# Performance work log

Measured on AMD Instinct MI355X. Metric: run time of the kernel, lower is better.

Reference implementation:

```python
import jax, jax.numpy as jnp
import numpy as np

H = 8  # num_heads, fixed in the module


def setup_inputs() -> dict:
    key = jax.random.key(0)
    ks = jax.random.split(key, 26)
    C = 256          # hidden_dim
    K = 16           # num_corners
    B = 8            # images
    P = 64           # proposals per image
    N = B * P        # total proposals
    Hf = Wf = 14     # feature map HxW (T = 196 keys per proposal)
    Hq = Wq = 10     # query grid (S = 100 queries)
    s = 1.0 / np.sqrt(C)

    def w(k, shape):
        return jax.random.normal(k, shape, jnp.float32) * s

    return {
        "features": jax.random.normal(ks[0], (N, C, Hf, Wf), jnp.float32),
        "query_features": jax.random.normal(ks[1], (B, C, Hq, Wq), jnp.float32),
        # self-attention params (torch MHA: y = x @ W.T + b)
        "wq_s": w(ks[2], (C, C)), "wk_s": w(ks[3], (C, C)), "wv_s": w(ks[4], (C, C)),
        "bq_s": jnp.zeros((C,), jnp.float32), "bk_s": jnp.zeros((C,), jnp.float32), "bv_s": jnp.zeros((C,), jnp.float32),
        "wo_s": w(ks[5], (C, C)), "bo_s": jnp.zeros((C,), jnp.float32),
        # cross-attention params
        "wq_c": w(ks[6], (C, C)), "wk_c": w(ks[7], (C, C)), "wv_c": w(ks[8], (C, C)),
        "bq_c": jnp.zeros((C,), jnp.float32), "bk_c": jnp.zeros((C,), jnp.float32), "bv_c": jnp.zeros((C,), jnp.float32),
        "wo_c": w(ks[9], (C, C)), "bo_c": jnp.zeros((C,), jnp.float32),
        # polygon MLP head
        "w1": w(ks[10], (C, C)), "b1": jnp.zeros((C,), jnp.float32),
        "w2": w(ks[11], (2 * K, C)), "b2": jnp.zeros((2 * K,), jnp.float32),
        # score head
        "ws": w(ks[12], (1, C)), "bs": jnp.zeros((1,), jnp.float32),
    }


def _forward(features, query_features,
             wq_s, wk_s, wv_s, bq_s, bk_s, bv_s, wo_s, bo_s,
             wq_c, wk_c, wv_c, bq_c, bk_c, bv_c, wo_c, bo_c,
             w1, b1, w2, b2, ws, bs):
    B, C = query_features.shape[0], query_features.shape[1]
    dh = C // H
    scale = 1.0 / jnp.sqrt(jnp.asarray(dh, jnp.float32))

    # query_features: (B,C,Hq,Wq) -> (S,B,C)
    qf = query_features.reshape(B, C, -1).transpose(2, 0, 1)
    S = qf.shape[0]

    # ---- self-attention over queries ----
    q = (qf @ wq_s.T + bq_s).reshape(S, B, H, dh)
    k = (qf @ wk_s.T + bk_s).reshape(S, B, H, dh)
    v = (qf @ wv_s.T + bv_s).reshape(S, B, H, dh)
    att = jax.nn.softmax(jnp.einsum('sbhd,tbhd->bhst', q, k) * scale, axis=-1)
    qsa = jnp.einsum('bhst,tbhd->sbhd', att, v).reshape(S, B, C) @ wo_s.T + bo_s  # (S,B,C)

    # features: (N,C,Hf,Wf) -> (B,P,T,C) with T=Hf*Wf, P=N//B
    N = features.shape[0]
    P = N // B
    feats = features.reshape(N, C, -1).transpose(0, 2, 1).reshape(B, P, -1, C)

    # ---- cross-attention: same (S,C) query broadcast over P proposals ----
    qc = (qsa @ wq_c.T + bq_c).reshape(S, B, H, dh)
    kc = (feats @ wk_c.T + bk_c).reshape(B, P, -1, H, dh)
    vc = (feats @ wv_c.T + bv_c).reshape(B, P, -1, H, dh)
    sc = jnp.einsum('sbhd,bpthd->bphst', qc, kc) * scale  # (B,P,H,S,T)
    a = jax.nn.softmax(sc, axis=-1)
    o = jnp.einsum('bphst,bpthd->bpshd', a, vc).reshape(B, P, S, C) @ wo_c.T + bo_c  # (B,P,S,C)

    # ---- heads, then mean over the S query positions ----
    h1 = jax.nn.relu(o @ w1.T + b1)
    polygons = (h1 @ w2.T + b2).mean(axis=2).reshape(N, -1)          # (N, 2K)
    scores = jax.nn.sigmoid(o @ ws.T + bs).mean(axis=2).reshape(N, 1)  # (N, 1)
    return polygons, scores


def reference(features, query_features,
              wq_s, wk_s, wv_s, bq_s, bk_s, bv_s, wo_s, bo_s,
              wq_c, wk_c, wv_c, bq_c, bk_c, bv_c, wo_c, bo_c,
              w1, b1, w2, b2, ws, bs):
    return _forward(features, query_features,
                    wq_s, wk_s, wv_s, bq_s, bk_s, bv_s, wo_s, bo_s,
                    wq_c, wk_c, wv_c, bq_c, bk_c, bv_c, wo_c, bo_c,
                    w1, b1, w2, b2, ws, bs)
```

## Files before the change

kernel.cpp:

```cpp
#include <hip/hip_runtime.h>
#include <hip/hip_bf16.h>


typedef __attribute__((ext_vector_type(8))) short bf16x8;
typedef __attribute__((ext_vector_type(4))) float f32x4;

__device__ __forceinline__ float bf2f(ushort u) {
    union { float f; uint u32; } v; v.u32 = ((uint)u) << 16; return v.f;
}
__device__ __forceinline__ ushort f2bf(float f) {
    union { float f; uint u; } v; v.f = f;
    uint r = v.u + 0x7FFF + ((v.u >> 16) & 1);
    return (ushort)(r >> 16);
}
__device__ __forceinline__ uint pk2(float a, float b) {
    __hip_bfloat162 h = __float22bfloat162_rn(make_float2(a, b));
    union { __hip_bfloat162 h2; uint u; } c; c.h2 = h; return c.u;
}
__device__ __forceinline__ f32x4 MFMA(bf16x8 a, bf16x8 b, f32x4 c) {
    return __builtin_amdgcn_mfma_f32_16x16x32_bf16(a, b, c, 0, 0, 0);
}

#define SCALE_DH 0.17677669529663687f

#define TOTALW (2337 * 256)
#define QCPN   (8 * 8 * 112 * 32)
#define NBIAS  2337

__global__ void prep_kernel(const float* w0, const float* w1_, const float* w2_,
                            const float* w3, const float* w4, const float* w5,
                            const float* w6, const float* w7, const float* w8,
                            const float* w9, const float* w10,
                            const float* b0, const float* b1_, const float* b2_,
                            const float* b3, const float* b4, const float* b5,
                            const float* b6, const float* b7, const float* b8,
                            const float* b9, const float* b10,
                            ushort* wbf, float* bias, ushort* qcp)
{
    for (size_t i = blockIdx.x * blockDim.x + threadIdx.x;
         i < (size_t)TOTALW + QCPN + NBIAS; i += (size_t)gridDim.x * blockDim.x) {
        if (i < TOTALW) {
            int row = (int)(i >> 8), col = (int)(i & 255);
            const float* sp; int base;
            if      (row < 256)  { sp = w0;  base = 0; }
            else if (row < 512)  { sp = w1_; base = 256; }
            else if (row < 768)  { sp = w2_; base = 512; }
            else if (row < 1024) { sp = w3;  base = 768; }
            else if (row < 1280) { sp = w4;  base = 1024; }
            else if (row < 1536) { sp = w5;  base = 1280; }
            else if (row < 1792) { sp = w6;  base = 1536; }
            else if (row < 2048) { sp = w7;  base = 1792; }
            else if (row < 2304) { sp = w8;  base = 2048; }
            else if (row < 2336) { sp = w9;  base = 2304; }
            else                 { sp = w10; base = 2336; }
            wbf[i] = f2bf(sp[(size_t)(row - base) * 256 + col]);
        } else if (i < (size_t)TOTALW + QCPN) {
            qcp[i - TOTALW] = 0;
        } else {
            int idx = (int)(i - TOTALW - QCPN);
            const float* sp; int base;
            if      (idx < 256)  { sp = b0;  base = 0; }
            else if (idx < 512)  { sp = b1_; base = 256; }
            else if (idx < 768)  { sp = b2_; base = 512; }
            else if (idx < 1024) { sp = b3;  base = 768; }
            else if (idx < 1280) { sp = b4;  base = 1024; }
            else if (idx < 1536) { sp = b5;  base = 1280; }
            else if (idx < 1792) { sp = b6;  base = 1536; }
            else if (idx < 2048) { sp = b7;  base = 1792; }
            else if (idx < 2304) { sp = b8;  base = 2048; }
            else if (idx < 2336) { sp = b9;  base = 2304; }
            else                 { sp = b10; base = 2336; }
            bias[idx] = sp[idx - base];
        }
    }
}

__global__ __launch_bounds__(256)
void wcomb(const float* wq_c, const float* wo_s, const float* bq_c,
           const float* bo_s, const float* bo_c, const float* wsc,
           const float* bs, ushort* wbf, float* bias)
{
    __shared__ float row[256];
    int i = blockIdx.x, k = threadIdx.x;
    row[k] = wq_c[(size_t)i * 256 + k];
    __syncthreads();
    float acc = 0.f;
    for (int j = 0; j < 256; ++j)
        acc = fmaf(row[j], wo_s[(size_t)j * 256 + k], acc);
    wbf[(size_t)(1024 + i) * 256 + k] = f2bf(acc);
    if (k == 0) {
        float s = bq_c[i];
        for (int j = 0; j < 256; ++j) s += row[j] * bo_s[j];
        bias[1024 + i] = s;
    }
    if (i == 0 && k == 1) {
        float s = bs[0];
        for (int j = 0; j < 256; ++j) s += bo_c[j] * wsc[j];
        bias[2336] = s;
    }
}

template<int ASRC, int GS, int EPI>
__global__ __launch_bounds__(256)
void gemm_rows(const void* Aptr, const ushort* Wall, const float* Ball,
               ushort* Out, int M, int Wrow0, int Brow0, int ldo)
{
    __shared__ ushort As[64 * 40];
    __shared__ ushort Bs[128 * 40];
    int tid = threadIdx.x;
    int lane = tid & 63, w = tid >> 6;
    int lr = lane & 15, lg = lane >> 4;
    int r0 = blockIdx.x * 64;
    int j0 = blockIdx.y * 128;

    f32x4 acc[4][2];
    #pragma unroll
    for (int mt = 0; mt < 4; ++mt)
        #pragma unroll
        for (int nt = 0; nt < 2; ++nt) { f32x4 z = {0.f,0.f,0.f,0.f}; acc[mt][nt] = z; }

    for (int ks = 0; ks < 8; ++ks) {
        int c0 = ks * 32;
        {
            int i = tid >> 2, q = tid & 3;
            int r = r0 + i;
            if (ASRC == 0) {
                uint4 v = make_uint4(0u,0u,0u,0u);
                if (r < M) v = *(const uint4*)((const ushort*)Aptr + (size_t)r * 256 + c0 + q * 8);
                *(uint4*)(&As[i * 40 + q * 8]) = v;
            } else {
                uint u[4] = {0u,0u,0u,0u};
                if (r < M) {
                    int g = r / GS, o = r - g * GS;
                    const float* src = (const float*)Aptr + (size_t)g * 256 * GS + o;
                    #pragma unroll
                    for (int k2 = 0; k2 < 4; ++k2) {
                        ushort a0 = f2bf(src[(size_t)(c0 + q * 8 + 2 * k2)     * GS]);
                        ushort a1 = f2bf(src[(size_t)(c0 + q * 8 + 2 * k2 + 1) * GS]);
                        u[k2] = (uint)a0 | ((uint)a1 << 16);
                    }
                }
                *(uint4*)(&As[i * 40 + q * 8]) = make_uint4(u[0], u[1], u[2], u[3]);
            }
        }
        {
            int jj = tid >> 1, half = tid & 1;
            const ushort* src = Wall + (size_t)(Wrow0 + j0 + jj) * 256 + c0 + half * 16;
            ushort* dst = &Bs[jj * 40 + half * 16];
            *(uint4*)(dst)     = *(const uint4*)(src);
            *(uint4*)(dst + 8) = *(const uint4*)(src + 8);
        }
        __syncthreads();
        bf16x8 bfr[2];
        #pragma unroll
        for (int nt = 0; nt < 2; ++nt)
            bfr[nt] = *(const bf16x8*)(&Bs[(w * 32 + nt * 16 + lr) * 40 + lg * 8]);
        #pragma unroll
        for (int mt = 0; mt < 4; ++mt) {
            bf16x8 afr = *(const bf16x8*)(&As[(mt * 16 + lr) * 40 + lg * 8]);
            acc[mt][0] = MFMA(afr, bfr[0], acc[mt][0]);
            acc[mt][1] = MFMA(afr, bfr[1], acc[mt][1]);
        }
        __syncthreads();
    }
    #pragma unroll
    for (int mt = 0; mt < 4; ++mt) {
        #pragma unroll
        for (int nt = 0; nt < 2; ++nt) {
            int jc = j0 + w * 32 + nt * 16 + lr;
            float bias = Ball[Brow0 + jc];
            #pragma unroll
            for (int rg = 0; rg < 4; ++rg) {
                int r = r0 + mt * 16 + lg * 4 + rg;
                if (r >= M) continue;
                float vv = acc[mt][nt][rg] + bias;
                if (EPI == 0) {
                    Out[(size_t)r * ldo + jc] = f2bf(vv);
                } else {
                    int b = r / 100, s = r - b * 100;
                    int h = jc >> 5, d = jc & 31;
                    Out[(((size_t)(b * 8 + h)) * 112 + s) * 32 + d] = f2bf(vv * SCALE_DH);
                }
            }
        }
    }
}

__global__ __launch_bounds__(128)
void self_attn(const ushort* qkv, ushort* sav)
{
    __shared__ float kls[100][33];
    __shared__ float vls[100][33];
    __shared__ float sls[100][101];
    int bh = blockIdx.x; int b = bh >> 3, h = bh & 7;
    int tid = threadIdx.x;
    for (int idx = tid; idx < 100 * 32; idx += 128) {
        int t = idx >> 5, d = idx & 31;
        kls[t][d] = bf2f(qkv[((size_t)(b * 100 + t)) * 768 + 256 + h * 32 + d]);
        vls[t][d] = bf2f(qkv[((size_t)(b * 100 + t)) * 768 + 512 + h * 32 + d]);
    }
    __syncthreads();
    if (tid < 100) {
        int s = tid;
        float q[32];
        #pragma unroll
        for (int d = 0; d < 32; ++d)
            q[d] = bf2f(qkv[((size_t)(b * 100 + s)) * 768 + h * 32 + d]) * SCALE_DH;
        float mx = -1e30f;
        for (int t = 0; t < 100; ++t) {
            float sc = 0.f;
            #pragma unroll
            for (int d = 0; d < 32; ++d) sc += q[d] * kls[t][d];
            sls[s][t] = sc; mx = fmaxf(mx, sc);
        }
        float sum = 0.f;
        for (int t = 0; t < 100; ++t) {
            float p = __expf(sls[s][t] - mx);
            sls[s][t] = p; sum += p;
        }
        float inv = 1.f / sum;
        float acc2[32];
        #pragma unroll
        for (int d = 0; d < 32; ++d) acc2[d] = 0.f;
        for (int t = 0; t < 100; ++t) {
            float pv = sls[s][t];
            #pragma unroll
            for (int d = 0; d < 32; ++d) acc2[d] += pv * vls[t][d];
        }
        #pragma unroll
        for (int d = 0; d < 32; ++d)
            sav[((size_t)(b * 100 + s)) * 256 + h * 32 + d] = f2bf(acc2[d] * inv);
    }
}

__global__ __launch_bounds__(512, 2)
void kvproj(const float* features, const ushort* Wall, const float* Ball,
            ushort* kc, ushort* vc, int n_base)
{
    __shared__ ushort featT[224 * 264];
    int tid = threadIdx.x;
    int lane = tid & 63, w = tid >> 6;
    int lr = lane & 15, lg = lane >> 4;
    int nl = blockIdx.x;
    int n  = n_base + nl;
    const float* fb = features + (size_t)n * 256 * 196;

    bf16x8 af[4][8];
    #pragma unroll
    for (int m = 0; m < 4; ++m) {
        int row = ((m < 2) ? 1280 : 1536) + w * 32 + (m & 1) * 16 + lr;
        #pragma unroll
        for (int ks = 0; ks < 8; ++ks)
            af[m][ks] = *(const bf16x8*)(Wall + (size_t)row * 256 + ks * 32 + lg * 8);
    }
    float biask0 = Ball[1280 + w * 32 + lr];
    float biask1 = Ball[1296 + w * 32 + lr];
    float biasv0 = Ball[1536 + w * 32 + lr];
    float biasv1 = Ball[1552 + w * 32 + lr];

    #pragma unroll
    for (int it = 0; it < 7; ++it) {
        int idx = tid + it * 512;
        if (idx < 3136) {
            int cg = idx / 49, tq = idx - cg * 49;
            const float* p = fb + (size_t)(cg * 4) * 196 + tq * 4;
            float4 v0 = *(const float4*)(p);
            float4 v1 = *(const float4*)(p + 196);
            float4 v2 = *(const float4*)(p + 392);
            float4 v3 = *(const float4*)(p + 588);
            #pragma unroll
            for (int j = 0; j < 4; ++j) {
                float e0 = (j == 0) ? v0.x : (j == 1) ? v0.y : (j == 2) ? v0.z : v0.w;
                float e1 = (j == 0) ? v1.x : (j == 1) ? v1.y : (j == 2) ? v1.z : v1.w;
                float e2 = (j == 0) ? v2.x : (j == 1) ? v2.y : (j == 2) ? v2.z : v2.w;
                float e3 = (j == 0) ? v3.x : (j == 1) ? v3.y : (j == 2) ? v3.z : v3.w;
                uint2 pr;
                pr.x = pk2(e0, e1);
                pr.y = pk2(e2, e3);
                *(uint2*)(&featT[(tq * 4 + j) * 264 + cg * 4]) = pr;
            }
        }
    }
    for (int idx = tid; idx < 12 * 264; idx += 512)
        featT[196 * 264 + idx] = 0;
    __syncthreads();

    for (int tt = 0; tt < 13; ++tt) {
        bf16x8 a8[8];
        #pragma unroll
        for (int ks = 0; ks < 8; ++ks)
            a8[ks] = *(const bf16x8*)(&featT[(tt * 16 + lr) * 264 + ks * 32 + lg * 8]);
        f32x4 acc[4];
        #pragma unroll
        for (int m = 0; m < 4; ++m) { f32x4 z = {0.f,0.f,0.f,0.f}; acc[m] = z; }
        #pragma unroll
        for (int ks = 0; ks < 8; ++ks)
            #pragma unroll
            for (int m = 0; m < 4; ++m)
                acc[m] = MFMA(a8[ks], af[m][ks], acc[m]);

        int tb = tt * 16 + lg * 4;
        #pragma unroll
        for (int rg = 0; rg < 4; ++rg) {
            int t = tb + rg;
            if (t < 196) {
                kc[((size_t)nl * 224 + t) * 256 + w * 32 + lr]      = f2bf(acc[0][rg] + biask0);
                kc[((size_t)nl * 224 + t) * 256 + w * 32 + 16 + lr] = f2bf(acc[1][rg] + biask1);
            }
        }
        if (tb < 196) {
            size_t vb0 = ((size_t)nl * 256 + w * 32 + lr) * 224 + tb;
            size_t vb1 = ((size_t)nl * 256 + w * 32 + 16 + lr) * 224 + tb;
            uint a01 = pk2(acc[2][0] + biasv0, acc[2][1] + biasv0);
            uint a23 = pk2(acc[2][2] + biasv0, acc[2][3] + biasv0);
            uint b01 = pk2(acc[3][0] + biasv1, acc[3][1] + biasv1);
            uint b23 = pk2(acc[3][2] + biasv1, acc[3][3] + biasv1);
            *(uint*)(vc + vb0)     = a01;
            *(uint*)(vc + vb0 + 2) = a23;
            *(uint*)(vc + vb1)     = b01;
            *(uint*)(vc + vb1 + 2) = b23;
        }
    }
}

__global__ __launch_bounds__(512, 2)
void attn_fuse(const ushort* qcp, const ushort* kc, const ushort* vc,
               const ushort* Wall, const float* Ball, float* outp, int n_base)
{
    __shared__ char smem[130816];
    ushort* OL     = (ushort*)smem;
    float* hbar    = (float*)(smem + 59392);
    float* scb     = (float*)(smem + 60416);
    float* sc_part = (float*)(smem + 60864);
    float* pp      = (float*)(smem + 64448);
    ushort* O2     = (ushort*)(smem + 71680);

    int tid = threadIdx.x;
    int lane = tid & 63; int w = tid >> 6;
    int lr = lane & 15, lg = lane >> 4;
    int nl = blockIdx.x; int n = n_base + nl;
    int b = n >> 6;
    const ushort* kcn = kc + (size_t)nl * 224 * 256;
    const ushort* vcn = vc + (size_t)nl * 256 * 224;

    bf16x8 qf[7];
    #pragma unroll
    for (int mt = 0; mt < 7; ++mt)
        qf[mt] = *(const bf16x8*)(qcp + ((((size_t)(b * 8 + w)) * 112 + mt * 16 + lr) * 32 + lg * 8));

    bf16x8 ones;
    #pragma unroll
    for (int j = 0; j < 8; ++j) ones[j] = (short)0x3F80;

    f32x4 o_acc[7][2], l_acc[7];
    #pragma unroll
    for (int mt = 0; mt < 7; ++mt) {
        f32x4 z = {0.f,0.f,0.f,0.f};
        o_acc[mt][0] = z; o_acc[mt][1] = z; l_acc[mt] = z;
    }

    const ushort* kbase = kcn + (size_t)lr * 256 + w * 32 + lg * 8;
    const ushort* vrow0 = vcn + ((size_t)(w * 32 + lr)) * 224;
    const ushort* vrow1 = vcn + ((size_t)(w * 32 + 16 + lr)) * 224;

    bf16x8 k0[3], k1[3];
    uint2 va[3], vb[3], vcq[3], vd[3];
    #pragma unroll
    for (int pc = 0; pc < 2; ++pc) {
        int t0n = pc * 32;
        k0[pc] = *(const bf16x8*)(kbase + (size_t)t0n * 256);
        k1[pc] = *(const bf16x8*)(kbase + (size_t)(t0n + 16) * 256);
        va[pc]  = *(const uint2*)(vrow0 + t0n + 4 * lg);
        vb[pc]  = *(const uint2*)(vrow0 + t0n + 16 + 4 * lg);
        vcq[pc] = *(const uint2*)(vrow1 + t0n + 4 * lg);
        vd[pc]  = *(const uint2*)(vrow1 + t0n + 16 + 4 * lg);
    }

    #pragma unroll
    for (int ch = 0; ch < 7; ++ch) {
        const int cur = ch % 3;
        int t0 = ch * 32;
        if (ch + 2 < 7) {
            const int nx = (ch + 2) % 3;
            int t0n = (ch + 2) * 32;
            k0[nx] = *(const bf16x8*)(kbase + (size_t)t0n * 256);
            k1[nx] = *(const bf16x8*)(kbase + (size_t)(t0n + 16) * 256);
            va[nx]  = *(const uint2*)(vrow0 + t0n + 4 * lg);
            vb[nx]  = *(const uint2*)(vrow0 + t0n + 16 + 4 * lg);
            vcq[nx] = *(const uint2*)(vrow1 + t0n + 4 * lg);
            vd[nx]  = *(const uint2*)(vrow1 + t0n + 16 + 4 * lg);
            if (t0n == 192) {
                uint2 zz = make_uint2(0u, 0u);
                vb[nx] = zz; vd[nx] = zz;
                if (lg) { va[nx] = zz; vcq[nx] = zz; }
            }
        }
        union { uint4 q; bf16x8 v; } u0, u1;
        u0.q = make_uint4(va[cur].x, va[cur].y, vb[cur].x, vb[cur].y);
        u1.q = make_uint4(vcq[cur].x, vcq[cur].y, vd[cur].x, vd[cur].y);
        bool mA[4], mB[4];
        #pragma unroll
        for (int r = 0; r < 4; ++r) {
            mA[r] = (t0 + 4 * lg + r)      >= 196;
            mB[r] = (t0 + 16 + 4 * lg + r) >= 196;
        }
        __builtin_amdgcn_s_setprio(1);
        #pragma unroll
        for (int mt = 0; mt < 7; ++mt) {
            f32x4 z = {0.f,0.f,0.f,0.f};
            f32x4 s0 = MFMA(k0[cur], qf[mt], z);
            f32x4 s1 = MFMA(k1[cur], qf[mt], z);
            float p00 = mA[0] ? 0.f : __expf(s0[0]);
            float p01 = mA[1] ? 0.f : __expf(s0[1]);
            float p02 = mA[2] ? 0.f : __expf(s0[2]);
            float p03 = mA[3] ? 0.f : __expf(s0[3]);
            float p10 = mB[0] ? 0.f : __expf(s1[0]);
            float p11 = mB[1] ? 0.f : __expf(s1[1]);
            float p12 = mB[2] ? 0.f : __expf(s1[2]);
            float p13 = mB[3] ? 0.f : __expf(s1[3]);
            union { uint4 q; bf16x8 v; } pu;
            pu.q.x = pk2(p00, p01);
            pu.q.y = pk2(p02, p03);
            pu.q.z = pk2(p10, p11);
            pu.q.w = pk2(p12, p13);
            o_acc[mt][0] = MFMA(pu.v, u0.v, o_acc[mt][0]);
            o_acc[mt][1] = MFMA(pu.v, u1.v, o_acc[mt][1]);
            l_acc[mt]    = MFMA(pu.v, ones, l_acc[mt]);
        }
        __builtin_amdgcn_s_setprio(0);
    }

    #pragma unroll
    for (int mt = 0; mt < 7; ++mt) {
        #pragma unroll
        for (int r = 0; r < 4; ++r) {
            float inv = 1.f / l_acc[mt][r];
            int srow = mt * 16 + lg * 4 + r;
            OL[srow * 264 + w * 32 + lr]      = f2bf(o_acc[mt][0][r] * inv);
            OL[srow * 264 + w * 32 + 16 + lr] = f2bf(o_acc[mt][1][r] * inv);
        }
    }
    __syncthreads();

    {
        f32x4 a2[7][2];
        #pragma unroll
        for (int mt = 0; mt < 7; ++mt) {
            f32x4 z = {0.f,0.f,0.f,0.f}; a2[mt][0] = z; a2[mt][1] = z;
        }
        for (int ks = 0; ks < 8; ++ks) {
            int c0 = ks * 32;
            bf16x8 bw0 = *(const bf16x8*)(Wall + (size_t)(1792 + w * 32 + lr) * 256 + c0 + lg * 8);
            bf16x8 bw1 = *(const bf16x8*)(Wall + (size_t)(1792 + w * 32 + 16 + lr) * 256 + c0 + lg * 8);
            #pragma unroll
            for (int mt = 0; mt < 7; ++mt) {
                bf16x8 afr = *(const bf16x8*)(&OL[(mt * 16 + lr) * 264 + c0 + lg * 8]);
                a2[mt][0] = MFMA(afr, bw0, a2[mt][0]);
                a2[mt][1] = MFMA(afr, bw1, a2[mt][1]);
            }
        }
        float wscA = bf2f(Wall[(size_t)2336 * 256 + w * 32 + lr]);
        float wscB = bf2f(Wall[(size_t)2336 * 256 + w * 32 + 16 + lr]);
        #pragma unroll
        for (int mt = 0; mt < 7; ++mt) {
            float sv0 = a2[mt][0][0] * wscA + a2[mt][1][0] * wscB;
            float sv1 = a2[mt][0][1] * wscA + a2[mt][1][1] * wscB;
            float sv2 = a2[mt][0][2] * wscA + a2[mt][1][2] * wscB;
            float sv3 = a2[mt][0][3] * wscA + a2[mt][1][3] * wscB;
            sv0 += __shfl_xor(sv0, 1); sv0 += __shfl_xor(sv0, 2);
            sv0 += __shfl_xor(sv0, 4); sv0 += __shfl_xor(sv0, 8);
            sv1 += __shfl_xor(sv1, 1); sv1 += __shfl_xor(sv1, 2);
            sv1 += __shfl_xor(sv1, 4); sv1 += __shfl_xor(sv1, 8);
            sv2 += __shfl_xor(sv2, 1); sv2 += __shfl_xor(sv2, 2);
            sv2 += __shfl_xor(sv2, 4); sv2 += __shfl_xor(sv2, 8);
            sv3 += __shfl_xor(sv3, 1); sv3 += __shfl_xor(sv3, 2);
            sv3 += __shfl_xor(sv3, 4); sv3 += __shfl_xor(sv3, 8);
            if (lr == 0) {
                int sb = w * 112 + mt * 16 + lg * 4;
                sc_part[sb]     = sv0;
                sc_part[sb + 1] = sv1;
                sc_part[sb + 2] = sv2;
                sc_part[sb + 3] = sv3;
            }
        }
        float biasA = Ball[1792 + w * 32 + lr];
        float biasB = Ball[1792 + w * 32 + 16 + lr];
        #pragma unroll
        for (int mt = 0; mt < 7; ++mt)
            #pragma unroll
            for (int r = 0; r < 4; ++r) {
                int srow = mt * 16 + lg * 4 + r;
                O2[srow * 264 + w * 32 + lr]      = f2bf(a2[mt][0][r] + biasA);
                O2[srow * 264 + w * 32 + 16 + lr] = f2bf(a2[mt][1][r] + biasB);
            }
    }
    __syncthreads();

    {
        f32x4 a2[7][2];
        #pragma unroll
        for (int mt = 0; mt < 7; ++mt) {
            f32x4 z = {0.f,0.f,0.f,0.f}; a2[mt][0] = z; a2[mt][1] = z;
        }
        for (int ks = 0; ks < 8; ++ks) {
            int c0 = ks * 32;
            bf16x8 bw0 = *(const bf16x8*)(Wall + (size_t)(2048 + w * 32 + lr) * 256 + c0 + lg * 8);
            bf16x8 bw1 = *(const bf16x8*)(Wall + (size_t)(2048 + w * 32 + 16 + lr) * 256 + c0 + lg * 8);
            #pragma unroll
            for (int mt = 0; mt < 7; ++mt) {
                bf16x8 afr = *(const bf16x8*)(&O2[(mt * 16 + lr) * 264 + c0 + lg * 8]);
                a2[mt][0] = MFMA(afr, bw0, a2[mt][0]);
                a2[mt][1] = MFMA(afr, bw1, a2[mt][1]);
            }
        }
        float biasA = Ball[2048 + w * 32 + lr];
        float biasB = Ball[2048 + w * 32 + 16 + lr];
        float hA = 0.f, hB = 0.f;
        #pragma unroll
        for (int mt = 0; mt < 7; ++mt)
            #pragma unroll
            for (int r = 0; r < 4; ++r) {
                int srow = mt * 16 + lg * 4 + r;
                if (srow < 100) {
                    float vA = a2[mt][0][r] + biasA; vA = vA > 0.f ? vA : 0.f;
                    float vB = a2[mt][1][r] + biasB; vB = vB > 0.f ? vB : 0.f;
                    hA += vA; hB += vB;
                }
            }
        hA += __shfl_xor(hA, 16); hA += __shfl_xor(hA, 32);
        hB += __shfl_xor(hB, 16); hB += __shfl_xor(hB, 32);
        if (lg == 0) {
            hbar[w * 32 + lr]      = hA * 0.01f;
            hbar[w * 32 + 16 + lr] = hB * 0.01f;
        }
        if (tid < 100) {
            float s = 0.f;
            #pragma unroll
            for (int ww = 0; ww < 8; ++ww) s += sc_part[ww * 112 + tid];
            s += Ball[2336];
            scb[tid] = 1.f / (1.f + __expf(-s));
        }
    }
    __syncthreads();

    if (tid < 256) {
        int g = tid >> 5, k = tid & 31;
        float s = 0.f;
        #pragma unroll
        for (int c2 = 0; c2 < 32; ++c2)
            s += hbar[g * 32 + c2] * bf2f(Wall[(size_t)(2304 + k) * 256 + g * 32 + c2]);
        pp[tid] = s;
    }
    if (tid == 320) {
        float s = 0.f;
        for (int i2 = 0; i2 < 100; ++i2) s += scb[i2];
        outp[16384 + n] = s * 0.01f;
    }
    __syncthreads();
    if (tid < 32) {
        float s = Ball[2304 + tid];
        #pragma unroll
        for (int g = 0; g < 8; ++g) s += pp[g * 32 + tid];
        outp[(size_t)n * 32 + tid] = s;
    }
}

extern "C" void kernel_launch(void* const* d_in, const int* in_sizes, int n_in,
                              void* d_out, int out_size, void* d_ws, size_t ws_size,
                              hipStream_t stream)
{
    const float* features = (const float*)d_in[0];
    const float* qfeat    = (const float*)d_in[1];
    char* ws = (char*)d_ws;

    ushort* wbf  = (ushort*)ws;
    float*  bias = (float*)(ws + 1196544);
    ushort* qkv  = (ushort*)(ws + 1206016);
    ushort* sav  = (ushort*)(ws + 2434816);
    ushort* qcp  = (ushort*)(ws + 3254016);
    ushort* kvb  = (ushort*)(ws + 3712768);

    prep_kernel<<<dim3(512), dim3(256), 0, stream>>>(
        (const float*)d_in[2], (const float*)d_in[3], (const float*)d_in[4],
        (const float*)d_in[8], (const float*)d_in[10], (const float*)d_in[11],
        (const float*)d_in[12], (const float*)d_in[16], (const float*)d_in[18],
        (const float*)d_in[20], (const float*)d_in[22],
        (const float*)d_in[5], (const float*)d_in[6], (const float*)d_in[7],
        (const float*)d_in[9], (const float*)d_in[13], (const float*)d_in[14],
        (const float*)d_in[15], (const float*)d_in[17], (const float*)d_in[19],
        (const float*)d_in[21], (const float*)d_in[23],
        wbf, bias, qcp);

    wcomb<<<dim3(256), dim3(256), 0, stream>>>(
        (const float*)d_in[10], (const float*)d_in[8],
        (const float*)d_in[13], (const float*)d_in[9],
        (const float*)d_in[17], (const float*)d_in[22],
        (const float*)d_in[23], wbf, bias);

    gemm_rows<1, 100, 0><<<dim3(13, 6), dim3(256), 0, stream>>>(
        qfeat, wbf, bias, qkv, 800, 0, 0, 768);
    self_attn<<<dim3(64), dim3(128), 0, stream>>>(qkv, sav);
    gemm_rows<0, 1, 1><<<dim3(13, 2), dim3(256), 0, stream>>>(
        sav, wbf, bias, qcp, 800, 1024, 1024, 0);

    const size_t per_n = 229376;
    long avail = (long)ws_size - 3712768L;
    int Np = 512;
    if (avail < (long)(per_n * 512)) {
        Np = (int)(avail / (long)per_n);
        if (Np < 1) Np = 1;
    }
    ushort* kcb = kvb;
    ushort* vcb = kvb + (size_t)Np * 224 * 256;
    float* outp = (float*)d_out;
    for (int n0 = 0; n0 < 512; n0 += Np) {
        int cnt = (512 - n0 < Np) ? (512 - n0) : Np;
        kvproj<<<dim3(cnt), dim3(512), 0, stream>>>(features, wbf, bias, kcb, vcb, n0);
        attn_fuse<<<dim3(cnt), dim3(512), 0, stream>>>(qcp, kcb, vcb, wbf, bias, outp, n0);
    }
}
```

Measured before the change: 199.8 us.

## Split feature staging in two halves and prefetch second half during first MFMA tiles

```diff
diff --git a/kernel.cpp b/kernel.cpp
--- a/kernel.cpp
+++ b/kernel.cpp
@@ -258,34 +258,7 @@
     float biasv0 = Ball[1536 + w * 32 + lr];
     float biasv1 = Ball[1552 + w * 32 + lr];
 
-    #pragma unroll
-    for (int it = 0; it < 7; ++it) {
-        int idx = tid + it * 512;
-        if (idx < 3136) {
-            int cg = idx / 49, tq = idx - cg * 49;
-            const float* p = fb + (size_t)(cg * 4) * 196 + tq * 4;
-            float4 v0 = *(const float4*)(p);
-            float4 v1 = *(const float4*)(p + 196);
-            float4 v2 = *(const float4*)(p + 392);
-            float4 v3 = *(const float4*)(p + 588);
-            #pragma unroll
-            for (int j = 0; j < 4; ++j) {
-                float e0 = (j == 0) ? v0.x : (j == 1) ? v0.y : (j == 2) ? v0.z : v0.w;
-                float e1 = (j == 0) ? v1.x : (j == 1) ? v1.y : (j == 2) ? v1.z : v1.w;
-                float e2 = (j == 0) ? v2.x : (j == 1) ? v2.y : (j == 2) ? v2.z : v2.w;
-                float e3 = (j == 0) ? v3.x : (j == 1) ? v3.y : (j == 2) ? v3.z : v3.w;
-                uint2 pr;
-                pr.x = pk2(e0, e1);
-                pr.y = pk2(e2, e3);
-                *(uint2*)(&featT[(tq * 4 + j) * 264 + cg * 4]) = pr;
-            }
-        }
-    }
-    for (int idx = tid; idx < 12 * 264; idx += 512)
-        featT[196 * 264 + idx] = 0;
-    __syncthreads();
-
-    for (int tt = 0; tt < 13; ++tt) {
+    auto do_tile = [&](int tt) {
         bf16x8 a8[8];
         #pragma unroll
         for (int ks = 0; ks < 8; ++ks)
@@ -320,7 +293,103 @@
             *(uint*)(vc + vb1)     = b01;
             *(uint*)(vc + vb1 + 2) = b23;
         }
-    }
+    };
+
+    #pragma unroll
+    for (int it = 0; it < 4; ++it) {
+        int idx = tid + it * 512;
+        if (idx < 1792) {
+            int cg = idx / 28, tq = idx - cg * 28;
+            const float* p = fb + (size_t)(cg * 4) * 196 + tq * 4;
+            float4 v0 = *(const float4*)(p);
+            float4 v1 = *(const float4*)(p + 196);
+            float4 v2 = *(const float4*)(p + 392);
+            float4 v3 = *(const float4*)(p + 588);
+            #pragma unroll
+            for (int j = 0; j < 4; ++j) {
+                float e0 = (j == 0) ? v0.x : (j == 1) ? v0.y : (j == 2) ? v0.z : v0.w;
+                float e1 = (j == 0) ? v1.x : (j == 1) ? v1.y : (j == 2) ? v1.z : v1.w;
+                float e2 = (j == 0) ? v2.x : (j == 1) ? v2.y : (j == 2) ? v2.z : v2.w;
+                float e3 = (j == 0) ? v3.x : (j == 1) ? v3.y : (j == 2) ? v3.z : v3.w;
+                uint2 pr;
+                pr.x = pk2(e0, e1);
+                pr.y = pk2(e2, e3);
+                *(uint2*)(&featT[(tq * 4 + j) * 264 + cg * 4]) = pr;
+            }
+        }
+    }
+    __syncthreads();
+
+    float4 pre0[4], pre1[4], pre2[4];
+    {
+        int idx = tid;
+        {
+            int cg = idx / 21, tq2 = idx - cg * 21;
+            const float* p = fb + (size_t)(cg * 4) * 196 + 112 + tq2 * 4;
+            pre0[0] = *(const float4*)(p);
+            pre0[1] = *(const float4*)(p + 196);
+            pre0[2] = *(const float4*)(p + 392);
+            pre0[3] = *(const float4*)(p + 588);
+        }
+        idx = tid + 512;
+        {
+            int cg = idx / 21, tq2 = idx - cg * 21;
+            const float* p = fb + (size_t)(cg * 4) * 196 + 112 + tq2 * 4;
+            pre1[0] = *(const float4*)(p);
+            pre1[1] = *(const float4*)(p + 196);
+            pre1[2] = *(const float4*)(p + 392);
+            pre1[3] = *(const float4*)(p + 588);
+        }
+        idx = tid + 1024;
+        if (idx < 1344) {
+            int cg = idx / 21, tq2 = idx - cg * 21;
+            const float* p = fb + (size_t)(cg * 4) * 196 + 112 + tq2 * 4;
+            pre2[0] = *(const float4*)(p);
+            pre2[1] = *(const float4*)(p + 196);
+            pre2[2] = *(const float4*)(p + 392);
+            pre2[3] = *(const float4*)(p + 588);
+        }
+    }
+
+    for (int tt = 0; tt < 7; ++tt) do_tile(tt);
+
+    #pragma unroll
+    for (int it = 0; it < 3; ++it) {
+        int idx = tid + it * 512;
+        if (idx < 1344) {
+            int cg = idx / 21, tq2 = idx - cg * 21;
+            int trow = 112 + tq2 * 4;
+            #pragma unroll
+            for (int j = 0; j < 4; ++j) {
+                float e0, e1, e2, e3;
+                if (it == 0) {
+                    e0 = (j == 0) ? pre0[0].x : (j == 1) ? pre0[0].y : (j == 2) ? pre0[0].z : pre0[0].w;
+                    e1 = (j == 0) ? pre0[1].x : (j == 1) ? pre0[1].y : (j == 2) ? pre0[1].z : pre0[1].w;
+                    e2 = (j == 0) ? pre0[2].x : (j == 1) ? pre0[2].y : (j == 2) ? pre0[2].z : pre0[2].w;
+                    e3 = (j == 0) ? pre0[3].x : (j == 1) ? pre0[3].y : (j == 2) ? pre0[3].z : pre0[3].w;
+                } else if (it == 1) {
+                    e0 = (j == 0) ? pre1[0].x : (j == 1) ? pre1[0].y : (j == 2) ? pre1[0].z : pre1[0].w;
+                    e1 = (j == 0) ? pre1[1].x : (j == 1) ? pre1[1].y : (j == 2) ? pre1[1].z : pre1[1].w;
+                    e2 = (j == 0) ? pre1[2].x : (j == 1) ? pre1[2].y : (j == 2) ? pre1[2].z : pre1[2].w;
+                    e3 = (j == 0) ? pre1[3].x : (j == 1) ? pre1[3].y : (j == 2) ? pre1[3].z : pre1[3].w;
+                } else {
+                    e0 = (j == 0) ? pre2[0].x : (j == 1) ? pre2[0].y : (j == 2) ? pre2[0].z : pre2[0].w;
+                    e1 = (j == 0) ? pre2[1].x : (j == 1) ? pre2[1].y : (j == 2) ? pre2[1].z : pre2[1].w;
+                    e2 = (j == 0) ? pre2[2].x : (j == 1) ? pre2[2].y : (j == 2) ? pre2[2].z : pre2[2].w;
+                    e3 = (j == 0) ? pre2[3].x : (j == 1) ? pre2[3].y : (j == 2) ? pre2[3].z : pre2[3].w;
+                }
+                uint2 pr;
+                pr.x = pk2(e0, e1);
+                pr.y = pk2(e2, e3);
+                *(uint2*)(&featT[(trow + j) * 264 + cg * 4]) = pr;
+            }
+        }
+    }
+    for (int idx = tid; idx < 12 * 264; idx += 512)
+        featT[196 * 264 + idx] = 0;
+    __syncthreads();
+
+    for (int tt = 7; tt < 13; ++tt) do_tile(tt);
 }
 
 __global__ __launch_bounds__(512, 2)
```

New measurement: 201.7 us. About the same (+1.0%).

## Fuse K/V projection into cross-attention kernel with double-buffered feature tiles

Applied to the files above, without the earlier changes.

```diff
diff --git a/kernel.cpp b/kernel.cpp
--- a/kernel.cpp
+++ b/kernel.cpp
@@ -234,100 +234,14 @@
 }
 
 __global__ __launch_bounds__(512, 2)
-void kvproj(const float* features, const ushort* Wall, const float* Ball,
-            ushort* kc, ushort* vc, int n_base)
-{
-    __shared__ ushort featT[224 * 264];
-    int tid = threadIdx.x;
-    int lane = tid & 63, w = tid >> 6;
-    int lr = lane & 15, lg = lane >> 4;
-    int nl = blockIdx.x;
-    int n  = n_base + nl;
-    const float* fb = features + (size_t)n * 256 * 196;
-
-    bf16x8 af[4][8];
-    #pragma unroll
-    for (int m = 0; m < 4; ++m) {
-        int row = ((m < 2) ? 1280 : 1536) + w * 32 + (m & 1) * 16 + lr;
-        #pragma unroll
-        for (int ks = 0; ks < 8; ++ks)
-            af[m][ks] = *(const bf16x8*)(Wall + (size_t)row * 256 + ks * 32 + lg * 8);
-    }
-    float biask0 = Ball[1280 + w * 32 + lr];
-    float biask1 = Ball[1296 + w * 32 + lr];
-    float biasv0 = Ball[1536 + w * 32 + lr];
-    float biasv1 = Ball[1552 + w * 32 + lr];
-
-    #pragma unroll
-    for (int it = 0; it < 7; ++it) {
-        int idx = tid + it * 512;
-        if (idx < 3136) {
-            int cg = idx / 49, tq = idx - cg * 49;
-            const float* p = fb + (size_t)(cg * 4) * 196 + tq * 4;
-            float4 v0 = *(const float4*)(p);
-            float4 v1 = *(const float4*)(p + 196);
-            float4 v2 = *(const float4*)(p + 392);
-            float4 v3 = *(const float4*)(p + 588);
-            #pragma unroll
-            for (int j = 0; j < 4; ++j) {
-                float e0 = (j == 0) ? v0.x : (j == 1) ? v0.y : (j == 2) ? v0.z : v0.w;
-                float e1 = (j == 0) ? v1.x : (j == 1) ? v1.y : (j == 2) ? v1.z : v1.w;
-                float e2 = (j == 0) ? v2.x : (j == 1) ? v2.y : (j == 2) ? v2.z : v2.w;
-                float e3 = (j == 0) ? v3.x : (j == 1) ? v3.y : (j == 2) ? v3.z : v3.w;
-                uint2 pr;
-                pr.x = pk2(e0, e1);
-                pr.y = pk2(e2, e3);
-                *(uint2*)(&featT[(tq * 4 + j) * 264 + cg * 4]) = pr;
-            }
-        }
-    }
-    for (int idx = tid; idx < 12 * 264; idx += 512)
-        featT[196 * 264 + idx] = 0;
-    __syncthreads();
-
-    for (int tt = 0; tt < 13; ++tt) {
-        bf16x8 a8[8];
-        #pragma unroll
-        for (int ks = 0; ks < 8; ++ks)
-            a8[ks] = *(const bf16x8*)(&featT[(tt * 16 + lr) * 264 + ks * 32 + lg * 8]);
-        f32x4 acc[4];
-        #pragma unroll
-        for (int m = 0; m < 4; ++m) { f32x4 z = {0.f,0.f,0.f,0.f}; acc[m] = z; }
-        #pragma unroll
-        for (int ks = 0; ks < 8; ++ks)
-            #pragma unroll
-            for (int m = 0; m < 4; ++m)
-                acc[m] = MFMA(a8[ks], af[m][ks], acc[m]);
-
-        int tb = tt * 16 + lg * 4;
-        #pragma unroll
-        for (int rg = 0; rg < 4; ++rg) {
-            int t = tb + rg;
-            if (t < 196) {
-                kc[((size_t)nl * 224 + t) * 256 + w * 32 + lr]      = f2bf(acc[0][rg] + biask0);
-                kc[((size_t)nl * 224 + t) * 256 + w * 32 + 16 + lr] = f2bf(acc[1][rg] + biask1);
-            }
-        }
-        if (tb < 196) {
-            size_t vb0 = ((size_t)nl * 256 + w * 32 + lr) * 224 + tb;
-            size_t vb1 = ((size_t)nl * 256 + w * 32 + 16 + lr) * 224 + tb;
-            uint a01 = pk2(acc[2][0] + biasv0, acc[2][1] + biasv0);
-            uint a23 = pk2(acc[2][2] + biasv0, acc[2][3] + biasv0);
-            uint b01 = pk2(acc[3][0] + biasv1, acc[3][1] + biasv1);
-            uint b23 = pk2(acc[3][2] + biasv1, acc[3][3] + biasv1);
-            *(uint*)(vc + vb0)     = a01;
-            *(uint*)(vc + vb0 + 2) = a23;
-            *(uint*)(vc + vb1)     = b01;
-            *(uint*)(vc + vb1 + 2) = b23;
-        }
-    }
-}
-
-__global__ __launch_bounds__(512, 2)
-void attn_fuse(const ushort* qcp, const ushort* kc, const ushort* vc,
-               const ushort* Wall, const float* Ball, float* outp, int n_base)
+void fused_cross(const float* features, const ushort* qcp, const ushort* Wall,
+                 const float* Ball, float* outp)
 {
     __shared__ char smem[130816];
+    ushort* fT0 = (ushort*)smem;
+    ushort* fT1 = (ushort*)(smem + 16896);
+    ushort* Kp  = (ushort*)(smem + 33792);
+    ushort* Vp  = (ushort*)(smem + 54272);
     ushort* OL     = (ushort*)smem;
     float* hbar    = (float*)(smem + 59392);
     float* scb     = (float*)(smem + 60416);
@@ -338,10 +252,19 @@
     int tid = threadIdx.x;
     int lane = tid & 63; int w = tid >> 6;
     int lr = lane & 15, lg = lane >> 4;
-    int nl = blockIdx.x; int n = n_base + nl;
-    int b = n >> 6;
-    const ushort* kcn = kc + (size_t)nl * 224 * 256;
-    const ushort* vcn = vc + (size_t)nl * 256 * 224;
+    int n = blockIdx.x; int b = n >> 6;
+    const float* fb = features + (size_t)n * 256 * 196;
+    ushort* Kw = Kp + w * 1280;
+    ushort* Vw = Vp + w * 1280;
+
+    const ushort* wk0b = Wall + (size_t)(1280 + w * 32 + lr) * 256 + lg * 8;
+    const ushort* wk1b = Wall + (size_t)(1296 + w * 32 + lr) * 256 + lg * 8;
+    const ushort* wv0b = Wall + (size_t)(1536 + w * 32 + lr) * 256 + lg * 8;
+    const ushort* wv1b = Wall + (size_t)(1552 + w * 32 + lr) * 256 + lg * 8;
+    float bk0 = Ball[1280 + w * 32 + lr];
+    float bk1 = Ball[1296 + w * 32 + lr];
+    float bv0 = Ball[1536 + w * 32 + lr];
+    float bv1 = Ball[1552 + w * 32 + lr];
 
     bf16x8 qf[7];
     #pragma unroll
@@ -359,75 +282,144 @@
         o_acc[mt][0] = z; o_acc[mt][1] = z; l_acc[mt] = z;
     }
 
-    const ushort* kbase = kcn + (size_t)lr * 256 + w * 32 + lg * 8;
-    const ushort* vrow0 = vcn + ((size_t)(w * 32 + lr)) * 224;
-    const ushort* vrow1 = vcn + ((size_t)(w * 32 + 16 + lr)) * 224;
-
-    bf16x8 k0[3], k1[3];
-    uint2 va[3], vb[3], vcq[3], vd[3];
-    #pragma unroll
-    for (int pc = 0; pc < 2; ++pc) {
-        int t0n = pc * 32;
-        k0[pc] = *(const bf16x8*)(kbase + (size_t)t0n * 256);
-        k1[pc] = *(const bf16x8*)(kbase + (size_t)(t0n + 16) * 256);
-        va[pc]  = *(const uint2*)(vrow0 + t0n + 4 * lg);
-        vb[pc]  = *(const uint2*)(vrow0 + t0n + 16 + 4 * lg);
-        vcq[pc] = *(const uint2*)(vrow1 + t0n + 4 * lg);
-        vd[pc]  = *(const uint2*)(vrow1 + t0n + 16 + 4 * lg);
-    }
-
-    #pragma unroll
+    {
+        int c = tid >> 3, tq = tid & 7;
+        #pragma unroll
+        for (int i = 0; i < 4; ++i) {
+            int idx = tid + i * 512;
+            int cc = idx >> 3, tqq = idx & 7;
+            float4 v = *(const float4*)(fb + (size_t)cc * 196 + tqq * 4);
+            #pragma unroll
+            for (int k = 0; k < 4; ++k) {
+                int j = (k + tqq) & 3;
+                float e = (j == 0) ? v.x : (j == 1) ? v.y : (j == 2) ? v.z : v.w;
+                fT0[(tqq * 4 + j) * 264 + cc] = f2bf(e);
+            }
+        }
+        (void)c; (void)tq;
+    }
+    __syncthreads();
+
+    float4 pre[4];
     for (int ch = 0; ch < 7; ++ch) {
-        const int cur = ch % 3;
+        ushort* Fc = (ch & 1) ? fT1 : fT0;
+        ushort* Fn = (ch & 1) ? fT0 : fT1;
         int t0 = ch * 32;
-        if (ch + 2 < 7) {
-            const int nx = (ch + 2) % 3;
-            int t0n = (ch + 2) * 32;
-            k0[nx] = *(const bf16x8*)(kbase + (size_t)t0n * 256);
-            k1[nx] = *(const bf16x8*)(kbase + (size_t)(t0n + 16) * 256);
-            va[nx]  = *(const uint2*)(vrow0 + t0n + 4 * lg);
-            vb[nx]  = *(const uint2*)(vrow0 + t0n + 16 + 4 * lg);
-            vcq[nx] = *(const uint2*)(vrow1 + t0n + 4 * lg);
-            vd[nx]  = *(const uint2*)(vrow1 + t0n + 16 + 4 * lg);
-            if (t0n == 192) {
-                uint2 zz = make_uint2(0u, 0u);
-                vb[nx] = zz; vd[nx] = zz;
-                if (lg) { va[nx] = zz; vcq[nx] = zz; }
-            }
-        }
-        union { uint4 q; bf16x8 v; } u0, u1;
-        u0.q = make_uint4(va[cur].x, va[cur].y, vb[cur].x, vb[cur].y);
-        u1.q = make_uint4(vcq[cur].x, vcq[cur].y, vd[cur].x, vd[cur].y);
-        bool mA[4], mB[4];
-        #pragma unroll
-        for (int r = 0; r < 4; ++r) {
-            mA[r] = (t0 + 4 * lg + r)      >= 196;
-            mB[r] = (t0 + 16 + 4 * lg + r) >= 196;
-        }
-        __builtin_amdgcn_s_setprio(1);
-        #pragma unroll
-        for (int mt = 0; mt < 7; ++mt) {
-            f32x4 z = {0.f,0.f,0.f,0.f};
-            f32x4 s0 = MFMA(k0[cur], qf[mt], z);
-            f32x4 s1 = MFMA(k1[cur], qf[mt], z);
-            float p00 = mA[0] ? 0.f : __expf(s0[0]);
-            float p01 = mA[1] ? 0.f : __expf(s0[1]);
-            float p02 = mA[2] ? 0.f : __expf(s0[2]);
-            float p03 = mA[3] ? 0.f : __expf(s0[3]);
-            float p10 = mB[0] ? 0.f : __expf(s1[0]);
-            float p11 = mB[1] ? 0.f : __expf(s1[1]);
-            float p12 = mB[2] ? 0.f : __expf(s1[2]);
-            float p13 = mB[3] ? 0.f : __expf(s1[3]);
-            union { uint4 q; bf16x8 v; } pu;
-            pu.q.x = pk2(p00, p01);
-            pu.q.y = pk2(p02, p03);
-            pu.q.z = pk2(p10, p11);
-            pu.q.w = pk2(p12, p13);
-            o_acc[mt][0] = MFMA(pu.v, u0.v, o_acc[mt][0]);
-            o_acc[mt][1] = MFMA(pu.v, u1.v, o_acc[mt][1]);
-            l_acc[mt]    = MFMA(pu.v, ones, l_acc[mt]);
-        }
-        __builtin_amdgcn_s_setprio(0);
+
+        {
+            f32x4 aK[2][2], aV[2][2];
+            #pragma unroll
+            for (int m = 0; m < 2; ++m)
+                #pragma unroll
+                for (int nt = 0; nt < 2; ++nt) {
+                    f32x4 z = {0.f,0.f,0.f,0.f}; aK[m][nt] = z; aV[m][nt] = z;
+                }
+            #pragma unroll
+            for (int ks = 0; ks < 8; ++ks) {
+                bf16x8 wk0 = *(const bf16x8*)(wk0b + ks * 32);
+                bf16x8 wk1 = *(const bf16x8*)(wk1b + ks * 32);
+                bf16x8 wv0 = *(const bf16x8*)(wv0b + ks * 32);
+                bf16x8 wv1 = *(const bf16x8*)(wv1b + ks * 32);
+                #pragma unroll
+                for (int m = 0; m < 2; ++m) {
+                    bf16x8 afr = *(const bf16x8*)(&Fc[(m * 16 + lr) * 264 + ks * 32 + lg * 8]);
+                    aK[m][0] = MFMA(afr, wk0, aK[m][0]);
+                    aK[m][1] = MFMA(afr, wk1, aK[m][1]);
+                    aV[m][0] = MFMA(afr, wv0, aV[m][0]);
+                    aV[m][1] = MFMA(afr, wv1, aV[m][1]);
+                }
+            }
+            #pragma unroll
+            for (int m = 0; m < 2; ++m)
+                #pragma unroll
+                for (int nt = 0; nt < 2; ++nt) {
+                    float bk_ = nt ? bk1 : bk0;
+                    #pragma unroll
+                    for (int r = 0; r < 4; ++r)
+                        Kw[(m * 16 + lg * 4 + r) * 40 + nt * 16 + lr] = f2bf(aK[m][nt][r] + bk_);
+                }
+            #pragma unroll
+            for (int m = 0; m < 2; ++m)
+                #pragma unroll
+                for (int nt = 0; nt < 2; ++nt) {
+                    float bv_ = nt ? bv1 : bv0;
+                    uint p01 = pk2(aV[m][nt][0] + bv_, aV[m][nt][1] + bv_);
+                    uint p23 = pk2(aV[m][nt][2] + bv_, aV[m][nt][3] + bv_);
+                    ushort* dst = &Vw[(nt * 16 + lr) * 40 + m * 16 + lg * 4];
+                    *(uint*)(dst)     = p01;
+                    *(uint*)(dst + 2) = p23;
+                }
+        }
+
+        if (ch < 6) {
+            int t0n = t0 + 32;
+            #pragma unroll
+            for (int i = 0; i < 4; ++i) {
+                int idx = tid + i * 512;
+                int cc = idx >> 3, tqq = idx & 7;
+                int tg = t0n + tqq * 4;
+                float4 z = {0.f, 0.f, 0.f, 0.f};
+                pre[i] = (tg < 196) ? *(const float4*)(fb + (size_t)cc * 196 + tg) : z;
+            }
+        }
+
+        {
+            bf16x8 ck0 = *(const bf16x8*)(&Kw[lr * 40 + lg * 8]);
+            bf16x8 ck1 = *(const bf16x8*)(&Kw[(16 + lr) * 40 + lg * 8]);
+            uint2 a0 = *(const uint2*)(&Vw[lr * 40 + 4 * lg]);
+            uint2 a1 = *(const uint2*)(&Vw[lr * 40 + 16 + 4 * lg]);
+            uint2 b0 = *(const uint2*)(&Vw[(16 + lr) * 40 + 4 * lg]);
+            uint2 b1 = *(const uint2*)(&Vw[(16 + lr) * 40 + 16 + 4 * lg]);
+            union { uint4 q; bf16x8 v; } u0, u1;
+            u0.q = make_uint4(a0.x, a0.y, a1.x, a1.y);
+            u1.q = make_uint4(b0.x, b0.y, b1.x, b1.y);
+            bool mA[4], mB[4];
+            #pragma unroll
+            for (int r = 0; r < 4; ++r) {
+                mA[r] = (t0 + 4 * lg + r)      >= 196;
+                mB[r] = (t0 + 16 + 4 * lg + r) >= 196;
+            }
+            __builtin_amdgcn_s_setprio(1);
+            #pragma unroll
+            for (int mt = 0; mt < 7; ++mt) {
+                f32x4 z = {0.f,0.f,0.f,0.f};
+                f32x4 s0 = MFMA(ck0, qf[mt], z);
+                f32x4 s1 = MFMA(ck1, qf[mt], z);
+                float p00 = mA[0] ? 0.f : __expf(s0[0]);
+                float p01 = mA[1] ? 0.f : __expf(s0[1]);
+                float p02 = mA[2] ? 0.f : __expf(s0[2]);
+                float p03 = mA[3] ? 0.f : __expf(s0[3]);
+                float p10 = mB[0] ? 0.f : __expf(s1[0]);
+                float p11 = mB[1] ? 0.f : __expf(s1[1]);
+                float p12 = mB[2] ? 0.f : __expf(s1[2]);
+                float p13 = mB[3] ? 0.f : __expf(s1[3]);
+                union { uint4 q; bf16x8 v; } pu;
+                pu.q.x = pk2(p00, p01);
+                pu.q.y = pk2(p02, p03);
+                pu.q.z = pk2(p10, p11);
+                pu.q.w = pk2(p12, p13);
+                o_acc[mt][0] = MFMA(pu.v, u0.v, o_acc[mt][0]);
+                o_acc[mt][1] = MFMA(pu.v, u1.v, o_acc[mt][1]);
+                l_acc[mt]    = MFMA(pu.v, ones, l_acc[mt]);
+            }
+            __builtin_amdgcn_s_setprio(0);
+        }
+
+        if (ch < 6) {
+            #pragma unroll
+            for (int i = 0; i < 4; ++i) {
+                int idx = tid + i * 512;
+                int cc = idx >> 3, tqq = idx & 7;
+                #pragma unroll
+                for (int k = 0; k < 4; ++k) {
+                    int j = (k + tqq) & 3;
+                    float e = (j == 0) ? pre[i].x : (j == 1) ? pre[i].y
+                            : (j == 2) ? pre[i].z : pre[i].w;
+                    Fn[(tqq * 4 + j) * 264 + cc] = f2bf(e);
+                }
+            }
+        }
+        __syncthreads();
     }
 
     #pragma unroll
@@ -578,7 +570,6 @@
     ushort* qkv  = (ushort*)(ws + 1206016);
     ushort* sav  = (ushort*)(ws + 2434816);
     ushort* qcp  = (ushort*)(ws + 3254016);
-    ushort* kvb  = (ushort*)(ws + 3712768);
 
     prep_kernel<<<dim3(512), dim3(256), 0, stream>>>(
         (const float*)d_in[2], (const float*)d_in[3], (const float*)d_in[4],
@@ -603,19 +594,6 @@
     gemm_rows<0, 1, 1><<<dim3(13, 2), dim3(256), 0, stream>>>(
         sav, wbf, bias, qcp, 800, 1024, 1024, 0);
 
-    const size_t per_n = 229376;
-    long avail = (long)ws_size - 3712768L;
-    int Np = 512;
-    if (avail < (long)(per_n * 512)) {
-        Np = (int)(avail / (long)per_n);
-        if (Np < 1) Np = 1;
-    }
-    ushort* kcb = kvb;
-    ushort* vcb = kvb + (size_t)Np * 224 * 256;
-    float* outp = (float*)d_out;
-    for (int n0 = 0; n0 < 512; n0 += Np) {
-        int cnt = (512 - n0 < Np) ? (512 - n0) : Np;
-        kvproj<<<dim3(cnt), dim3(512), 0, stream>>>(features, wbf, bias, kcb, vcb, n0);
-        attn_fuse<<<dim3(cnt), dim3(512), 0, stream>>>(qcp, kcb, vcb, wbf, bias, outp, n0);
-    }
-}
+    fused_cross<<<dim3(512), dim3(512), 0, stream>>>(
+        features, qcp, wbf, bias, (float*)d_out);
+}
```

After: 275.3 us. 1.38x slower.
